# Performance work log

Hardware: AMD Instinct MI355X
Metric: run time of the kernel (lower is better)

The kernel has to match this reference:

```python
import jax, jax.numpy as jnp
import numpy as np

NUM_GRAPHS = 64  # len(torch.unique(batch)) in the original

def _glorot(k, shape):
    lim = float(np.sqrt(6.0 / (shape[0] + shape[1])))
    return jax.random.uniform(k, shape, jnp.float32, -lim, lim)

def setup_inputs() -> dict:
    key = jax.random.key(0)
    ks = jax.random.split(key, 16)
    N, E, F_IN, C, H = 100000, 1600000, 128, 500, 128
    x = jax.random.normal(ks[0], (N, F_IN), jnp.float32)
    edge_index = jax.random.randint(ks[1], (2, E), 0, N, jnp.int32)
    batch = jnp.sort(jax.random.randint(ks[2], (N,), 0, NUM_GRAPHS, jnp.int32))
    W1 = _glorot(ks[3], (F_IN, 64));  b1 = jnp.zeros((64,), jnp.float32)
    W2 = _glorot(ks[4], (64, 128));   b2 = jnp.zeros((128,), jnp.float32)
    W3 = _glorot(ks[5], (128, 256));  b3 = jnp.zeros((256,), jnp.float32)
    # LSTM params (PyTorch gate order i,f,g,o); b = b_ih + b_hh combined
    w_ih_f = _glorot(ks[6], (4 * H, 256)); w_hh_f = _glorot(ks[7], (4 * H, H))
    bias_f = jnp.zeros((4 * H,), jnp.float32)
    w_ih_b = _glorot(ks[8], (4 * H, 256)); w_hh_b = _glorot(ks[9], (4 * H, H))
    bias_b = jnp.zeros((4 * H,), jnp.float32)
    fc_w = _glorot(ks[10], (256, C)); fc_b = jnp.zeros((C,), jnp.float32)
    return dict(x=x, edge_index=edge_index, batch=batch,
                W1=W1, b1=b1, W2=W2, b2=b2, W3=W3, b3=b3,
                w_ih_f=w_ih_f, w_hh_f=w_hh_f, bias_f=bias_f,
                w_ih_b=w_ih_b, w_hh_b=w_hh_b, bias_b=bias_b,
                fc_w=fc_w, fc_b=fc_b)

def reference(x, W1, b1, W2, b2, W3, b3,
              w_ih_f, w_hh_f, bias_f, w_ih_b, w_hh_b, bias_b,
              fc_w, fc_b, edge_index, batch):
    N = x.shape[0]
    src, dst = edge_index[0], edge_index[1]
    # GCN symmetric norm with self-loops: deg = in-degree + 1
    deg = jnp.zeros((N,), x.dtype).at[dst].add(jnp.ones((src.shape[0],), x.dtype)) + 1.0
    dinv = jax.lax.rsqrt(deg)
    norm = (dinv[src] * dinv[dst])[:, None]      # [E,1]
    self_norm = (1.0 / deg)[:, None]             # [N,1]

    def gcn(h, W, b):
        h = h @ W                                # [N,out]
        agg = jnp.zeros_like(h).at[dst].add(h[src] * norm)
        return agg + h * self_norm + b

    h = jax.nn.relu(gcn(x, W1, b1))              # dropout p=0.2 is eval-mode identity
    h = jax.nn.relu(gcn(h, W2, b2))
    h = jax.nn.relu(gcn(h, W3, b3))              # [N,256]

    # global_mean_pool
    sums = jax.ops.segment_sum(h, batch, num_segments=NUM_GRAPHS)
    cnt = jax.ops.segment_sum(jnp.ones((N,), h.dtype), batch, num_segments=NUM_GRAPHS)
    pooled = sums / jnp.maximum(cnt, 1.0)[:, None]   # [B,256]

    # seq_len = num_graphs // len(unique(batch)) == 1 in the original
    seq = pooled[:, None, :]                     # [B,1,256]
    B, T, _ = seq.shape
    H = w_hh_f.shape[1]

    def run_lstm(s, w_ih, w_hh, bias):
        def step(carry, xt):
            hp, cp = carry
            g = xt @ w_ih.T + hp @ w_hh.T + bias
            i, f, gg, o = jnp.split(g, 4, axis=-1)
            c = jax.nn.sigmoid(f) * cp + jax.nn.sigmoid(i) * jnp.tanh(gg)
            hh = jax.nn.sigmoid(o) * jnp.tanh(c)
            return (hh, c), hh
        init = (jnp.zeros((B, H), s.dtype), jnp.zeros((B, H), s.dtype))
        _, hs = jax.lax.scan(step, init, jnp.swapaxes(s, 0, 1))
        return jnp.swapaxes(hs, 0, 1)            # [B,T,H]

    out_f = run_lstm(seq, w_ih_f, w_hh_f, bias_f)
    out_b = run_lstm(seq[:, ::-1, :], w_ih_b, w_hh_b, bias_b)[:, ::-1, :]
    lstm_out = jnp.concatenate([out_f, out_b], axis=-1)   # [B,T,2H]

    logits = lstm_out[:, -1, :] @ fc_w + fc_b
    return jax.nn.log_softmax(logits, axis=1)
```

## Files before the change

kernel.cpp:

```cpp
#include <hip/hip_runtime.h>
#include <cstdint>
#include <cstddef>

#define CDIV(a,b) (((a)+(b)-1)/(b))
constexpr int NG = 64;
constexpr int CAP = 64;
constexpr int RBITS = 9;
constexpr int NRMAX = 256;
constexpr int RCAP = 9216;

typedef _Float16 h4 __attribute__((ext_vector_type(4)));
typedef _Float16 h8 __attribute__((ext_vector_type(8)));
typedef float f4 __attribute__((ext_vector_type(4)));
typedef float f2 __attribute__((ext_vector_type(2)));

__device__ __forceinline__ void acc8(int2 v, float* a) {
  f2 p;
  p = __builtin_amdgcn_cvt_pk_f32_fp8(v.x, false); a[0] += p.x; a[1] += p.y;
  p = __builtin_amdgcn_cvt_pk_f32_fp8(v.x, true);  a[2] += p.x; a[3] += p.y;
  p = __builtin_amdgcn_cvt_pk_f32_fp8(v.y, false); a[4] += p.x; a[5] += p.y;
  p = __builtin_amdgcn_cvt_pk_f32_fp8(v.y, true);  a[6] += p.x; a[7] += p.y;
}
__device__ __forceinline__ int pack4(float x0, float x1, float x2, float x3) {
  int r = __builtin_amdgcn_cvt_pk_fp8_f32(x0, x1, 0, false);
  r = __builtin_amdgcn_cvt_pk_fp8_f32(x2, x3, r, true);
  return r;
}

__global__ void k_init(int* zp, long zn, unsigned char* Q0, unsigned char* Q1, int N) {
  long i = (long)blockIdx.x*blockDim.x + threadIdx.x;
  long stride = (long)gridDim.x*blockDim.x;
  for (; i < zn; i += stride) zp[i] = 0;
  if (blockIdx.x == 0) {
    int t = threadIdx.x;
    if (t < 64)       Q0[(size_t)N*64 + t] = 0;
    else if (t < 128) Q1[(size_t)N*64 + (t-64)] = 0;
    else              Q1[(size_t)N*128 + (t-128)] = 0;
  }
}

__global__ void k_wcvt_all(const float* __restrict__ W1, const float* __restrict__ W2,
                           const float* __restrict__ W3, _Float16* __restrict__ WT1,
                           _Float16* __restrict__ WT2, _Float16* __restrict__ WT3) {
  int idx = blockIdx.x*256 + threadIdx.x;
  if (idx < 8192) {
    int c = idx >> 7, k = idx & 127;
    WT1[idx] = (_Float16)W1[(size_t)k*64 + c];
  } else if (idx < 16384) {
    int j = idx - 8192;
    int c = j >> 6, k = j & 63;
    WT2[j] = (_Float16)W2[(size_t)k*128 + c];
  } else if (idx < 49152) {
    int j = idx - 16384;
    int c = j >> 7, k = j & 127;
    WT3[j] = (_Float16)W3[(size_t)k*256 + c];
  }
}

__global__ __launch_bounds__(256) void k_part(
    const int* __restrict__ src, const int* __restrict__ dst,
    int* __restrict__ rngcur, unsigned* __restrict__ part, int E) {
  __shared__ int hcnt[NRMAX], hbase[NRMAX], hfill[NRMAX];
  int tid = threadIdx.x;
  int base = blockIdx.x * 4096;
  hcnt[tid] = 0;
  __syncthreads();
  unsigned val[16]; int rr[16];
  #pragma unroll
  for (int u = 0; u < 16; u++) {
    int e = base + u*256 + tid;
    rr[u] = -1;
    if (e < E) {
      int s = src[e], d = dst[e];
      rr[u] = d >> RBITS;
      val[u] = ((unsigned)(d & ((1<<RBITS)-1)) << 17) | (unsigned)s;
      atomicAdd(&hcnt[rr[u]], 1);
    }
  }
  __syncthreads();
  hfill[tid] = 0;
  if (hcnt[tid]) hbase[tid] = atomicAdd(&rngcur[tid], hcnt[tid]);
  __syncthreads();
  #pragma unroll
  for (int u = 0; u < 16; u++) {
    if (rr[u] >= 0) {
      int p = hbase[rr[u]] + atomicAdd(&hfill[rr[u]], 1);
      if (p < RCAP) part[(size_t)rr[u]*RCAP + p] = val[u];
    }
  }
}

__global__ __launch_bounds__(512) void k_csr3(
    const unsigned* __restrict__ part, const int* __restrict__ rngcur,
    const int* __restrict__ batch, int* __restrict__ icnt, float* __restrict__ dinv,
    int* __restrict__ ecol, int* __restrict__ cnt_g, int N) {
  __shared__ unsigned sorted[RCAP];
  __shared__ int lcnt[512], lpos[512], lcur[512];
  __shared__ int wsum[8], hist[NG];
  int r = blockIdx.x;
  int tid = threadIdx.x;
  int cnt = min(rngcur[r], RCAP);
  int n0 = r << RBITS;
  int nn = min(512, N - n0);
  const unsigned* p = part + (size_t)r * RCAP;
  lcnt[tid] = 0; lcur[tid] = 0;
  if (tid < NG) hist[tid] = 0;
  __syncthreads();
  for (int i = tid; i < cnt; i += 512)
    atomicAdd(&lcnt[p[i] >> 17], 1);
  __syncthreads();
  {
    int lane = tid & 63, wv = tid >> 6;
    int s = lcnt[tid];
    #pragma unroll
    for (int off = 1; off < 64; off <<= 1) {
      int t = __shfl_up(s, off, 64);
      if (lane >= off) s += t;
    }
    if (lane == 63) wsum[wv] = s;
    __syncthreads();
    int add = 0;
    #pragma unroll
    for (int j = 0; j < 8; j++) if (j < wv) add += wsum[j];
    lpos[tid] = s + add;
  }
  __syncthreads();
  for (int i = tid; i < cnt; i += 512) {
    unsigned v = p[i];
    int d = v >> 17;
    int q = (lpos[d] - lcnt[d]) + atomicAdd(&lcur[d], 1);
    sorted[q] = v & 131071u;
  }
  if (tid < nn) {
    int c = min(lcnt[tid], CAP);
    icnt[n0 + tid] = c;
    dinv[n0 + tid] = rsqrtf((float)(c + 1));
    atomicAdd(&hist[batch[n0 + tid]], 1);
  }
  __syncthreads();
  if (tid < NG && hist[tid]) atomicAdd(&cnt_g[tid], hist[tid]);
  int wv = tid >> 6, lane = tid & 63;
  for (int i = wv; i < nn; i += 8) {
    int c = min(lcnt[i], CAP);
    int pc = (c + 15) & ~15;
    if (lane < pc) {
      int v = (lane < c) ? (int)sorted[lpos[i] - lcnt[i] + lane] : N;
      ecol[(size_t)(n0 + i)*CAP + lane] = v;
    }
  }
}

template<int F, bool L1>
__global__ __launch_bounds__(256) void k_gather_q(
    const unsigned char* __restrict__ y, unsigned char* __restrict__ z,
    const int* __restrict__ ecol, const int* __restrict__ icnt,
    const float* __restrict__ dinv, const float* __restrict__ bias, int n) {
  constexpr int LPN = F / 8;
  constexpr int NPW = 64 / LPN;
  int wid = (int)((blockIdx.x*(size_t)blockDim.x + threadIdx.x) >> 6);
  int lane = threadIdx.x & 63;
  int sub = lane / LPN;
  int li  = lane % LPN;
  int gw = wid * NPW + sub;
  if (gw >= n) return;
  float di = dinv[gw];
  float a[8] = {};
  { int2 v = *(const int2*)(y + (size_t)gw*F + li*8); acc8(v, a); }
  int padc = (icnt[gw] + 15) & ~15;
  const int* col = ecol + (size_t)gw * CAP;
  for (int k = 0; k < padc; k += 16) {
    int4 c0 = *(const int4*)&col[k];
    int4 c1 = *(const int4*)&col[k+4];
    int4 c2 = *(const int4*)&col[k+8];
    int4 c3 = *(const int4*)&col[k+12];
    int c[16] = {c0.x,c0.y,c0.z,c0.w, c1.x,c1.y,c1.z,c1.w,
                 c2.x,c2.y,c2.z,c2.w, c3.x,c3.y,c3.z,c3.w};
    int2 v[16];
    #pragma unroll
    for (int u = 0; u < 16; u++)
      v[u] = *(const int2*)(y + (size_t)c[u]*F + li*8);
    #pragma unroll
    for (int u = 0; u < 16; u++) acc8(v[u], a);
  }
  if constexpr (L1) {
    #pragma unroll
    for (int j = 0; j < 8; j++)
      a[j] = di * fmaxf(di*a[j] + bias[li*8 + j], 0.f);
  } else {
    #pragma unroll
    for (int j = 0; j < 8; j++) a[j] *= di;
  }
  int2 o;
  o.x = pack4(a[0], a[1], a[2], a[3]);
  o.y = pack4(a[4], a[5], a[6], a[7]);
  *(int2*)(z + (size_t)gw*F + li*8) = o;
}

template<int K, int CF, int EPI, bool AF32>
__global__ __launch_bounds__(256, 2) void k_mgemm(
    const void* __restrict__ Av, const _Float16* __restrict__ WT,
    const float* __restrict__ bias, unsigned char* __restrict__ C,
    int n, const int* __restrict__ batch, float* __restrict__ gsum,
    const float* __restrict__ rs) {
  constexpr int KS = K / 32;
  constexpr int NOUT = CF * 64;
  constexpr int LDA = K + 8;
  __shared__ __align__(16) _Float16 sA[64][LDA];
  __shared__ float red[4][256];
  __shared__ int sBatch[64];
  int tid = threadIdx.x;
  int row0 = blockIdx.x * 64;
  int lane = tid & 63, wv = tid >> 6;
  int grp = lane >> 4, l16 = lane & 15;
  int wcol0 = wv * (CF * 16);

  {
    int srow = tid >> 2;
    bool ok = (row0 + srow) < n;
    if constexpr (AF32) {
      const float* A = (const float*)Av;
      #pragma unroll
      for (int u = 0; u < K/16; u++) {
        int c4 = (tid & 3) + 4*u;
        float4 v = ok ? *(const float4*)(A + (size_t)(row0+srow)*K + c4*4)
                      : make_float4(0.f,0.f,0.f,0.f);
        h4 o; o.x=(_Float16)v.x; o.y=(_Float16)v.y; o.z=(_Float16)v.z; o.w=(_Float16)v.w;
        *(h4*)&sA[srow][c4*4] = o;
      }
    } else {
      const unsigned char* A = (const unsigned char*)Av;
      #pragma unroll
      for (int u = 0; u < K/32; u++) {
        int off = ((tid & 3) + 4*u) * 8;
        int2 v = ok ? *(const int2*)(A + (size_t)(row0+srow)*K + off) : make_int2(0,0);
        f2 p0 = __builtin_amdgcn_cvt_pk_f32_fp8(v.x, false);
        f2 p1 = __builtin_amdgcn_cvt_pk_f32_fp8(v.x, true);
        f2 p2 = __builtin_amdgcn_cvt_pk_f32_fp8(v.y, false);
        f2 p3 = __builtin_amdgcn_cvt_pk_f32_fp8(v.y, true);
        h8 o;
        o[0]=(_Float16)p0.x; o[1]=(_Float16)p0.y; o[2]=(_Float16)p1.x; o[3]=(_Float16)p1.y;
        o[4]=(_Float16)p2.x; o[5]=(_Float16)p2.y; o[6]=(_Float16)p3.x; o[7]=(_Float16)p3.y;
        *(h8*)&sA[srow][off] = o;
      }
    }
  }
  if constexpr (EPI == 2) {
    if (tid < 64) sBatch[tid] = (row0 + tid < n) ? batch[row0 + tid] : -1;
  }

  h8 bfrag[KS][CF];
  #pragma unroll
  for (int ks = 0; ks < KS; ks++)
    #pragma unroll
    for (int cf = 0; cf < CF; cf++) {
      int col = wcol0 + cf*16 + l16;
      bfrag[ks][cf] = *(const h8*)(WT + (size_t)col*K + ks*32 + grp*8);
    }

  f4 acc[4][CF] = {};
  __syncthreads();

  #pragma unroll
  for (int ks = 0; ks < KS; ks++) {
    h8 af[4];
    #pragma unroll
    for (int rf = 0; rf < 4; rf++)
      af[rf] = *(const h8*)&sA[rf*16 + l16][ks*32 + grp*8];
    #pragma unroll
    for (int rf = 0; rf < 4; rf++)
      #pragma unroll
      for (int cf = 0; cf < CF; cf++)
        acc[rf][cf] = __builtin_amdgcn_mfma_f32_16x16x32_f16(
            af[rf], bfrag[ks][cf], acc[rf][cf], 0, 0, 0);
  }

  if constexpr (EPI <= 1) {
    #pragma unroll
    for (int rf = 0; rf < 4; rf++) {
      #pragma unroll
      for (int r = 0; r < 4; r++) {
        int row = row0 + rf*16 + grp*4 + r;
        if (row < n) {
          float rsv = rs ? rs[row] : 1.f;
          #pragma unroll
          for (int cf = 0; cf < CF; cf++) {
            int col = wcol0 + cf*16 + l16;
            float v = acc[rf][cf][r];
            if constexpr (EPI == 1) v = fmaxf(v + bias[col], 0.f);
            v *= rsv;
            int b = __builtin_amdgcn_cvt_pk_fp8_f32(v, v, 0, false);
            C[(size_t)row*NOUT + col] = (unsigned char)(b & 0xff);
          }
        }
      }
    }
  } else {
    float bv[CF];
    #pragma unroll
    for (int cf = 0; cf < CF; cf++) bv[cf] = bias[wcol0 + cf*16 + l16];
    #pragma unroll
    for (int rf = 0; rf < 4; rf++)
      #pragma unroll
      for (int cf = 0; cf < CF; cf++)
        #pragma unroll
        for (int r = 0; r < 4; r++)
          acc[rf][cf][r] = fmaxf(acc[rf][cf][r] + bv[cf], 0.f);
    __syncthreads();
    int g0 = sBatch[0];
    int g1 = batch[min(row0 + 63, n - 1)];
    for (int g = g0; g <= g1; ++g) {
      float p[CF] = {};
      #pragma unroll
      for (int rf = 0; rf < 4; rf++)
        #pragma unroll
        for (int r = 0; r < 4; r++) {
          int lrow = rf*16 + grp*4 + r;
          bool m = (sBatch[lrow] == g);
          #pragma unroll
          for (int cf = 0; cf < CF; cf++)
            if (m) p[cf] += acc[rf][cf][r];
        }
      #pragma unroll
      for (int cf = 0; cf < CF; cf++)
        red[grp][wcol0 + cf*16 + l16] = p[cf];
      __syncthreads();
      if (tid < NOUT) {
        float s = red[0][tid] + red[1][tid] + red[2][tid] + red[3][tid];
        atomicAdd(&gsum[g*256 + tid], s);
      }
      __syncthreads();
    }
  }
}

__device__ __forceinline__ float sigm(float x) { return 1.f / (1.f + expf(-x)); }

__global__ __launch_bounds__(256) void k_gates(
    const float* __restrict__ gsum, const int* __restrict__ cnt_g,
    const float* __restrict__ wf, const float* __restrict__ bf,
    const float* __restrict__ wb, const float* __restrict__ bb,
    float* __restrict__ gates) {
  int g = blockIdx.y;
  int j0 = blockIdx.x * 64;
  int tid = threadIdx.x;
  __shared__ float pooled[256];
  float invc = 1.0f / fmaxf((float)cnt_g[g], 1.0f);
  pooled[tid] = gsum[g*256 + tid] * invc;
  __syncthreads();
  int jl = tid >> 2, ks = tid & 3;
  int j = j0 + jl;
  const float* wrow;
  float bias;
  if (j < 512) { wrow = wf + (size_t)j*256;        bias = bf[j]; }
  else         { wrow = wb + (size_t)(j-512)*256;  bias = bb[j-512]; }
  const float4* w4 = (const float4*)(wrow + ks*64);
  const float4* p4 = (const float4*)(&pooled[ks*64]);
  float acc = 0.f;
  #pragma unroll
  for (int i = 0; i < 16; i++) {
    float4 a = w4[i], b = p4[i];
    acc += a.x*b.x + a.y*b.y + a.z*b.z + a.w*b.w;
  }
  acc += __shfl_xor(acc, 1, 64);
  acc += __shfl_xor(acc, 2, 64);
  if (ks == 0) gates[(size_t)g*1024 + j] = acc + bias;
}

__global__ __launch_bounds__(256) void k_lstmfc(
    const float* __restrict__ gates, const float* __restrict__ fw,
    const float* __restrict__ fb, float* __restrict__ logits) {
  int g = blockIdx.y;
  int c0 = blockIdx.x * 125;
  int tid = threadIdx.x;
  __shared__ float gg[1024];
  __shared__ float lstm[256];
  __shared__ float sred[256];
  #pragma unroll
  for (int u = 0; u < 4; u++) gg[tid + u*256] = gates[(size_t)g*1024 + tid + u*256];
  __syncthreads();
  if (tid < 128) {
    float i = gg[tid], z = gg[256+tid], o = gg[384+tid];
    float cc = sigm(i)*tanhf(z);
    lstm[tid] = sigm(o)*tanhf(cc);
  } else {
    int u = tid - 128;
    float i = gg[512+u], z = gg[768+u], o = gg[896+u];
    float cc = sigm(i)*tanhf(z);
    lstm[128+u] = sigm(o)*tanhf(cc);
  }
  __syncthreads();
  int kh = tid >> 7;
  int cl = tid & 127;
  float acc = 0.f;
  if (cl < 125) {
    const float* fcol = fw + (size_t)kh*128*500 + (c0 + cl);
    #pragma unroll 8
    for (int k = 0; k < 128; k++)
      acc += lstm[kh*128 + k] * fcol[(size_t)k*500];
  }
  sred[tid] = acc;
  __syncthreads();
  if (tid < 125)
    logits[(size_t)g*500 + c0 + tid] = sred[tid] + sred[tid+128] + fb[c0 + tid];
}

__global__ __launch_bounds__(256) void k_smax(
    const float* __restrict__ logits, float* __restrict__ out) {
  int g = blockIdx.x, tid = threadIdx.x;
  __shared__ float sred[256];
  float l0 = logits[(size_t)g*500 + tid];
  float l1 = (tid < 244) ? logits[(size_t)g*500 + 256 + tid] : -1e30f;
  float m = fmaxf(l0, l1);
  sred[tid] = m; __syncthreads();
  for (int d = 128; d > 0; d >>= 1) {
    if (tid < d) sred[tid] = fmaxf(sred[tid], sred[tid+d]);
    __syncthreads();
  }
  float mx = sred[0]; __syncthreads();
  float s = expf(l0 - mx) + ((tid < 244) ? expf(l1 - mx) : 0.f);
  sred[tid] = s; __syncthreads();
  for (int d = 128; d > 0; d >>= 1) {
    if (tid < d) sred[tid] += sred[tid+d];
    __syncthreads();
  }
  float lse = logf(sred[0]) + mx;
  out[(size_t)g*500 + tid] = l0 - lse;
  if (tid < 244) out[(size_t)g*500 + 256 + tid] = l1 - lse;
}

extern "C" void kernel_launch(void* const* d_in, const int* in_sizes, int n_in,
                              void* d_out, int out_size, void* d_ws, size_t ws_size,
                              hipStream_t stream) {
  const float* x     = (const float*)d_in[0];
  const int*   ei    = (const int*)d_in[1];
  const int*   batch = (const int*)d_in[2];
  const float* W1 = (const float*)d_in[3];  const float* b1 = (const float*)d_in[4];
  const float* W2 = (const float*)d_in[5];  const float* b2 = (const float*)d_in[6];
  const float* W3 = (const float*)d_in[7];  const float* b3 = (const float*)d_in[8];
  const float* wf = (const float*)d_in[9];  const float* bf = (const float*)d_in[11];
  const float* wb = (const float*)d_in[12]; const float* bb = (const float*)d_in[14];
  const float* fw = (const float*)d_in[15]; const float* fb = (const float*)d_in[16];
  int N = in_sizes[2];
  int E = in_sizes[1] / 2;
  const int* src = ei;
  const int* dst = ei + E;
  int NR = CDIV(N, 1 << RBITS);

  char* w = (char*)d_ws;
  auto alloc = [&](size_t bytes) { char* p = w; w += (bytes + 255) / 256 * 256; return p; };
  int*   cnt_g  = (int*)  alloc(NG*4);
  int*   rngcur = (int*)  alloc(NRMAX*4);
  float* gsum   = (float*)alloc(NG*256*4);
  char*  zero_end = w;
  int*   icnt  = (int*)  alloc((size_t)N*4);
  float* dinv  = (float*)alloc((size_t)N*4);
  unsigned* part = (unsigned*)alloc((size_t)NR*RCAP*4);
  int*   ecol  = (int*)  alloc((size_t)N*CAP*4);
  unsigned char* Q0 = (unsigned char*)alloc(((size_t)N+1)*128);
  unsigned char* Q1 = (unsigned char*)alloc(((size_t)N+1)*128);
  _Float16* WT1 = (_Float16*)alloc(128*64*2);
  _Float16* WT2 = (_Float16*)alloc(64*128*2);
  _Float16* WT3 = (_Float16*)alloc(128*256*2);
  float* gates  = (float*)alloc((size_t)NG*1024*4);
  float* logits = (float*)alloc((size_t)NG*500*4);

  long zwords = (zero_end - (char*)cnt_g) / 4;
  k_init<<<64, 256, 0, stream>>>(cnt_g, zwords, Q0, Q1, N);
  k_wcvt_all<<<192, 256, 0, stream>>>(W1, W2, W3, WT1, WT2, WT3);
  k_part<<<CDIV(E,4096), 256, 0, stream>>>(src, dst, rngcur, part, E);
  k_csr3<<<NR, 512, 0, stream>>>(part, rngcur, batch, icnt, dinv, ecol, cnt_g, N);

  k_mgemm<128,1,0,true><<<CDIV(N,64), 256, 0, stream>>>(x, WT1, nullptr, Q0, N, nullptr, nullptr, dinv);
  k_gather_q<64,true><<<CDIV(N,32), 256, 0, stream>>>(Q0, Q1, ecol, icnt, dinv, b1, N);
  k_gather_q<64,false><<<CDIV(N,32), 256, 0, stream>>>(Q1, Q0, ecol, icnt, dinv, nullptr, N);
  k_mgemm<64,2,1,false><<<CDIV(N,64), 256, 0, stream>>>(Q0, WT2, b2, Q1, N, nullptr, nullptr, dinv);
  k_gather_q<128,false><<<CDIV(N,16), 256, 0, stream>>>(Q1, Q0, ecol, icnt, dinv, nullptr, N);
  k_mgemm<128,4,2,false><<<CDIV(N,64), 256, 0, stream>>>(Q0, WT3, b3, nullptr, N, batch, gsum, nullptr);
  k_gates<<<dim3(16, NG), 256, 0, stream>>>(gsum, cnt_g, wf, bf, wb, bb, gates);
  k_lstmfc<<<dim3(4, NG), 256, 0, stream>>>(gates, fw, fb, logits);
  k_smax<<<NG, 256, 0, stream>>>(logits, (float*)d_out);
}
```

Before: 203.2 us.

## Fuse neighbor gather into GEMM A-tile load and merge setup kernels

Two of the three standalone gather kernels are removed; the GEMM for layers 2 and 3 now performs the CSR neighbor aggregation itself while filling its shared-memory A tile, so the aggregated fp8 intermediate is never written to or re-read from global memory. The init, weight-conversion and edge-partition kernels are merged into a single launch, and zeroing moves to hipMemsetAsync, which cuts launch count. The fused gather runs with the GEMM's block shape and occupancy (launch bounds 256,2 with large shared arrays), which may hide gather latency less well than the dedicated gather kernels did. The sentinel zero row is now cleared in Q0 at N*128 instead of Q1, to match the new buffer roles.

Result: faster. 197.6 us (-2.8%).

```diff
diff --git a/kernel.cpp b/kernel.cpp
--- a/kernel.cpp
+++ b/kernel.cpp
@@ -27,42 +27,39 @@
   return r;
 }
 
-__global__ void k_init(int* zp, long zn, unsigned char* Q0, unsigned char* Q1, int N) {
-  long i = (long)blockIdx.x*blockDim.x + threadIdx.x;
-  long stride = (long)gridDim.x*blockDim.x;
-  for (; i < zn; i += stride) zp[i] = 0;
-  if (blockIdx.x == 0) {
-    int t = threadIdx.x;
-    if (t < 64)       Q0[(size_t)N*64 + t] = 0;
-    else if (t < 128) Q1[(size_t)N*64 + (t-64)] = 0;
-    else              Q1[(size_t)N*128 + (t-128)] = 0;
-  }
-}
-
-__global__ void k_wcvt_all(const float* __restrict__ W1, const float* __restrict__ W2,
-                           const float* __restrict__ W3, _Float16* __restrict__ WT1,
-                           _Float16* __restrict__ WT2, _Float16* __restrict__ WT3) {
-  int idx = blockIdx.x*256 + threadIdx.x;
-  if (idx < 8192) {
-    int c = idx >> 7, k = idx & 127;
-    WT1[idx] = (_Float16)W1[(size_t)k*64 + c];
-  } else if (idx < 16384) {
-    int j = idx - 8192;
-    int c = j >> 6, k = j & 63;
-    WT2[j] = (_Float16)W2[(size_t)k*128 + c];
-  } else if (idx < 49152) {
-    int j = idx - 16384;
-    int c = j >> 7, k = j & 127;
-    WT3[j] = (_Float16)W3[(size_t)k*256 + c];
-  }
-}
-
-__global__ __launch_bounds__(256) void k_part(
+__global__ __launch_bounds__(256) void k_comboA(
+    unsigned char* Q0, unsigned char* Q1, int N,
+    const float* __restrict__ W1, const float* __restrict__ W2,
+    const float* __restrict__ W3, _Float16* __restrict__ WT1,
+    _Float16* __restrict__ WT2, _Float16* __restrict__ WT3,
     const int* __restrict__ src, const int* __restrict__ dst,
     int* __restrict__ rngcur, unsigned* __restrict__ part, int E) {
+  int b = blockIdx.x;
+  int tid = threadIdx.x;
+  if (b == 0) {
+    if (tid < 64)       Q0[(size_t)N*64 + tid] = 0;
+    else if (tid < 128) Q1[(size_t)N*64 + (tid-64)] = 0;
+    else                Q0[(size_t)N*128 + (tid-128)] = 0;
+    return;
+  }
+  if (b < 193) {
+    int idx = (b-1)*256 + tid;
+    if (idx < 8192) {
+      int c = idx >> 7, k = idx & 127;
+      WT1[idx] = (_Float16)W1[(size_t)k*64 + c];
+    } else if (idx < 16384) {
+      int j = idx - 8192;
+      int c = j >> 6, k = j & 63;
+      WT2[j] = (_Float16)W2[(size_t)k*128 + c];
+    } else if (idx < 49152) {
+      int j = idx - 16384;
+      int c = j >> 7, k = j & 127;
+      WT3[j] = (_Float16)W3[(size_t)k*256 + c];
+    }
+    return;
+  }
   __shared__ int hcnt[NRMAX], hbase[NRMAX], hfill[NRMAX];
-  int tid = threadIdx.x;
-  int base = blockIdx.x * 4096;
+  int base = (b - 193) * 4096;
   hcnt[tid] = 0;
   __syncthreads();
   unsigned val[16]; int rr[16];
@@ -196,12 +193,13 @@
   *(int2*)(z + (size_t)gw*F + li*8) = o;
 }
 
-template<int K, int CF, int EPI, bool AF32>
+template<int K, int CF, int EPI, int GM>
 __global__ __launch_bounds__(256, 2) void k_mgemm(
     const void* __restrict__ Av, const _Float16* __restrict__ WT,
     const float* __restrict__ bias, unsigned char* __restrict__ C,
     int n, const int* __restrict__ batch, float* __restrict__ gsum,
-    const float* __restrict__ rs) {
+    const float* __restrict__ rs, const int* __restrict__ ecol,
+    const int* __restrict__ icnt, const float* __restrict__ dinvp) {
   constexpr int KS = K / 32;
   constexpr int NOUT = CF * 64;
   constexpr int LDA = K + 8;
@@ -214,34 +212,51 @@
   int grp = lane >> 4, l16 = lane & 15;
   int wcol0 = wv * (CF * 16);
 
-  {
+  if constexpr (GM == 0) {
+    const float* A = (const float*)Av;
     int srow = tid >> 2;
     bool ok = (row0 + srow) < n;
-    if constexpr (AF32) {
-      const float* A = (const float*)Av;
-      #pragma unroll
-      for (int u = 0; u < K/16; u++) {
-        int c4 = (tid & 3) + 4*u;
-        float4 v = ok ? *(const float4*)(A + (size_t)(row0+srow)*K + c4*4)
-                      : make_float4(0.f,0.f,0.f,0.f);
-        h4 o; o.x=(_Float16)v.x; o.y=(_Float16)v.y; o.z=(_Float16)v.z; o.w=(_Float16)v.w;
-        *(h4*)&sA[srow][c4*4] = o;
+    #pragma unroll
+    for (int u = 0; u < K/16; u++) {
+      int c4 = (tid & 3) + 4*u;
+      float4 v = ok ? *(const float4*)(A + (size_t)(row0+srow)*K + c4*4)
+                    : make_float4(0.f,0.f,0.f,0.f);
+      h4 o; o.x=(_Float16)v.x; o.y=(_Float16)v.y; o.z=(_Float16)v.z; o.w=(_Float16)v.w;
+      *(h4*)&sA[srow][c4*4] = o;
+    }
+  } else {
+    constexpr int SL = K / 8;
+    const unsigned char* Y = (const unsigned char*)Av;
+    for (int un = tid; un < 64*SL; un += 256) {
+      int row = un / SL, sl = un % SL;
+      int grow = row0 + row;
+      float a[8] = {};
+      if (grow < n) {
+        { int2 v0 = *(const int2*)(Y + (size_t)grow*K + sl*8); acc8(v0, a); }
+        int padc = (icnt[grow] + 15) & ~15;
+        const int* col = ecol + (size_t)grow * CAP;
+        for (int k = 0; k < padc; k += 16) {
+          int4 c0 = *(const int4*)&col[k];
+          int4 c1 = *(const int4*)&col[k+4];
+          int4 c2 = *(const int4*)&col[k+8];
+          int4 c3 = *(const int4*)&col[k+12];
+          int c[16] = {c0.x,c0.y,c0.z,c0.w, c1.x,c1.y,c1.z,c1.w,
+                       c2.x,c2.y,c2.z,c2.w, c3.x,c3.y,c3.z,c3.w};
+          int2 v[16];
+          #pragma unroll
+          for (int u = 0; u < 16; u++)
+            v[u] = *(const int2*)(Y + (size_t)c[u]*K + sl*8);
+          #pragma unroll
+          for (int u = 0; u < 16; u++) acc8(v[u], a);
+        }
+        float di = dinvp[grow];
+        #pragma unroll
+        for (int j = 0; j < 8; j++) a[j] *= di;
       }
-    } else {
-      const unsigned char* A = (const unsigned char*)Av;
-      #pragma unroll
-      for (int u = 0; u < K/32; u++) {
-        int off = ((tid & 3) + 4*u) * 8;
-        int2 v = ok ? *(const int2*)(A + (size_t)(row0+srow)*K + off) : make_int2(0,0);
-        f2 p0 = __builtin_amdgcn_cvt_pk_f32_fp8(v.x, false);
-        f2 p1 = __builtin_amdgcn_cvt_pk_f32_fp8(v.x, true);
-        f2 p2 = __builtin_amdgcn_cvt_pk_f32_fp8(v.y, false);
-        f2 p3 = __builtin_amdgcn_cvt_pk_f32_fp8(v.y, true);
-        h8 o;
-        o[0]=(_Float16)p0.x; o[1]=(_Float16)p0.y; o[2]=(_Float16)p1.x; o[3]=(_Float16)p1.y;
-        o[4]=(_Float16)p2.x; o[5]=(_Float16)p2.y; o[6]=(_Float16)p3.x; o[7]=(_Float16)p3.y;
-        *(h8*)&sA[srow][off] = o;
-      }
+      h8 o;
+      #pragma unroll
+      for (int j = 0; j < 8; j++) o[j] = (_Float16)a[j];
+      *(h8*)&sA[row][sl*8] = o;
     }
   }
   if constexpr (EPI == 2) {
@@ -445,6 +460,7 @@
   const int* src = ei;
   const int* dst = ei + E;
   int NR = CDIV(N, 1 << RBITS);
+  int NBPART = CDIV(E, 4096);
 
   char* w = (char*)d_ws;
   auto alloc = [&](size_t bytes) { char* p = w; w += (bytes + 255) / 256 * 256; return p; };
@@ -464,18 +480,19 @@
   float* gates  = (float*)alloc((size_t)NG*1024*4);
   float* logits = (float*)alloc((size_t)NG*500*4);
 
-  long zwords = (zero_end - (char*)cnt_g) / 4;
-  k_init<<<64, 256, 0, stream>>>(cnt_g, zwords, Q0, Q1, N);
-  k_wcvt_all<<<192, 256, 0, stream>>>(W1, W2, W3, WT1, WT2, WT3);
-  k_part<<<CDIV(E,4096), 256, 0, stream>>>(src, dst, rngcur, part, E);
+  size_t zbytes = (size_t)(zero_end - (char*)cnt_g);
+  hipMemsetAsync(cnt_g, 0, zbytes, stream);
+  k_comboA<<<193 + NBPART, 256, 0, stream>>>(Q0, Q1, N, W1, W2, W3, WT1, WT2, WT3,
+                                             src, dst, rngcur, part, E);
   k_csr3<<<NR, 512, 0, stream>>>(part, rngcur, batch, icnt, dinv, ecol, cnt_g, N);
 
-  k_mgemm<128,1,0,true><<<CDIV(N,64), 256, 0, stream>>>(x, WT1, nullptr, Q0, N, nullptr, nullptr, dinv);
+  k_mgemm<128,1,0,0><<<CDIV(N,64), 256, 0, stream>>>(x, WT1, nullptr, Q0, N,
+      nullptr, nullptr, dinv, nullptr, nullptr, nullptr);
   k_gather_q<64,true><<<CDIV(N,32), 256, 0, stream>>>(Q0, Q1, ecol, icnt, dinv, b1, N);
-  k_gather_q<64,false><<<CDIV(N,32), 256, 0, stream>>>(Q1, Q0, ecol, icnt, dinv, nullptr, N);
-  k_mgemm<64,2,1,false><<<CDIV(N,64), 256, 0, stream>>>(Q0, WT2, b2, Q1, N, nullptr, nullptr, dinv);
-  k_gather_q<128,false><<<CDIV(N,16), 256, 0, stream>>>(Q1, Q0, ecol, icnt, dinv, nullptr, N);
-  k_mgemm<128,4,2,false><<<CDIV(N,64), 256, 0, stream>>>(Q0, WT3, b3, nullptr, N, batch, gsum, nullptr);
+  k_mgemm<64,2,1,2><<<CDIV(N,64), 256, 0, stream>>>(Q1, WT2, b2, Q0, N,
+      nullptr, nullptr, dinv, ecol, icnt, dinv);
+  k_mgemm<128,4,2,2><<<CDIV(N,64), 256, 0, stream>>>(Q0, WT3, b3, nullptr, N,
+      batch, gsum, nullptr, ecol, icnt, dinv);
   k_gates<<<dim3(16, NG), 256, 0, stream>>>(gsum, cnt_g, wf, bf, wb, bb, gates);
   k_lstmfc<<<dim3(4, NG), 256, 0, stream>>>(gates, fw, fb, logits);
   k_smax<<<NG, 256, 0, stream>>>(logits, (float*)d_out);
```
